# Optimization experiments

Measured on AMD Instinct MI355X. Metric: run time of the kernel, lower is better.

## Reference

```python
import jax, jax.numpy as jnp
import numpy as np

N_NODES = 100000
N_EDGES = 2000000
F_IN = 32
HID = 32
N_CLASS = 40


def _gru_cell(m, h, wih, whh, bih, bhh):
    # torch.nn.GRUCell math; wih/whh: [3H, H_in], gates ordered r, z, n
    gi = m @ wih.T + bih
    gh = h @ whh.T + bhh
    i_r, i_z, i_n = jnp.split(gi, 3, axis=-1)
    h_r, h_z, h_n = jnp.split(gh, 3, axis=-1)
    r = jax.nn.sigmoid(i_r + h_r)
    z = jax.nn.sigmoid(i_z + h_z)
    n = jnp.tanh(i_n + r * h_n)
    return (1.0 - z) * n + z * h


def _gated_conv(x, edge_index, edge_weight, w_proj, w_msg, wih, whh, bih, bhh):
    h = x @ w_proj                                   # [N, out]
    msg = (h @ w_msg)[edge_index[0]] * edge_weight[:, None]  # gather src -> [E, out]
    agg = jax.ops.segment_sum(msg, edge_index[1], num_segments=N_NODES)  # scatter-add to dst
    return _gru_cell(agg, h, wih, whh, bih, bhh)


def setup_inputs() -> dict:
    key = jax.random.key(0)
    ks = jax.random.split(key, 16)
    s = 0.1
    return {
        "x": jax.random.normal(ks[0], (N_NODES, F_IN), jnp.float32),
        "edge_index": jax.random.randint(ks[1], (2, N_EDGES), 0, N_NODES, jnp.int64),
        "edge_weight": jax.random.uniform(ks[2], (N_EDGES,), jnp.float32),
        "W1_proj": jax.random.normal(ks[3], (F_IN, HID), jnp.float32) * s,
        "W1_msg": jax.random.normal(ks[4], (HID, HID), jnp.float32) * s,
        "gru1_wih": jax.random.normal(ks[5], (3 * HID, HID), jnp.float32) * s,
        "gru1_whh": jax.random.normal(ks[6], (3 * HID, HID), jnp.float32) * s,
        "gru1_bih": jax.random.normal(ks[7], (3 * HID,), jnp.float32) * s,
        "gru1_bhh": jax.random.normal(ks[8], (3 * HID,), jnp.float32) * s,
        "W2_proj": jax.random.normal(ks[9], (HID, N_CLASS), jnp.float32) * s,
        "W2_msg": jax.random.normal(ks[10], (N_CLASS, N_CLASS), jnp.float32) * s,
        "gru2_wih": jax.random.normal(ks[11], (3 * N_CLASS, N_CLASS), jnp.float32) * s,
        "gru2_whh": jax.random.normal(ks[12], (3 * N_CLASS, N_CLASS), jnp.float32) * s,
        "gru2_bih": jax.random.normal(ks[13], (3 * N_CLASS,), jnp.float32) * s,
        "gru2_bhh": jax.random.normal(ks[14], (3 * N_CLASS,), jnp.float32) * s,
    }


def reference(x, edge_index, edge_weight, W1_proj, W1_msg, gru1_wih, gru1_whh,
              gru1_bih, gru1_bhh, W2_proj, W2_msg, gru2_wih, gru2_whh,
              gru2_bih, gru2_bhh):
    # eval mode: dropout is identity
    h = _gated_conv(x, edge_index, edge_weight, W1_proj, W1_msg,
                    gru1_wih, gru1_whh, gru1_bih, gru1_bhh)
    h = jax.nn.relu(h)
    h = _gated_conv(h, edge_index, edge_weight, W2_proj, W2_msg,
                    gru2_wih, gru2_whh, gru2_bih, gru2_bhh)
    return jax.nn.log_softmax(h, axis=-1)
```

## Files before the change

### kernel.cpp

```cpp
#include <hip/hip_runtime.h>
#include <math.h>

#define NN 100000
#define NP 100032
#define NE 2000000
#define FIN 32
#define H 32
#define NC 40

#define NBK 196
#define BSH 9
#define CAP 11264
#define EPT 16
#define EPB (256 * EPT)

typedef _Float16 half_t;
typedef __attribute__((ext_vector_type(8))) _Float16 half8;
typedef __attribute__((ext_vector_type(4))) float f32x4;

__device__ __forceinline__ float sigm_(float x) {
    return 1.0f / (1.0f + __expf(-x));
}
__device__ __forceinline__ float tanh_(float x) {
    x = fminf(fmaxf(x, -20.0f), 20.0f);
    float e = __expf(2.0f * x);
    return (e - 1.0f) / (e + 1.0f);
}

__global__ __launch_bounds__(256) void kA_bucket(const int* __restrict__ ei,
                                                 const float* __restrict__ ew,
                                                 int* __restrict__ gcur,
                                                 long long* __restrict__ rec) {
    __shared__ long long recs[EPB];
    __shared__ int gdst[EPB];
    __shared__ int cnt[NBK], base[NBK], sofs[NBK];
    __shared__ int ssc[256];
    int tid = threadIdx.x;
    for (int i = tid; i < NBK; i += 256) cnt[i] = 0;
    __syncthreads();
    int e0 = blockIdx.x * EPB;
    int dcache[EPT];
#pragma unroll
    for (int i = 0; i < EPT; ++i) {
        int e = e0 + i * 256 + tid;
        dcache[i] = (e < NE) ? ei[NE + e] : -1;
        if (e < NE) atomicAdd(&cnt[dcache[i] >> BSH], 1);
    }
    __syncthreads();
    int cv = (tid < NBK) ? cnt[tid] : 0;
    ssc[tid] = cv;
    __syncthreads();
    for (int off = 1; off < 256; off <<= 1) {
        int v = (tid >= off) ? ssc[tid - off] : 0;
        __syncthreads();
        ssc[tid] += v;
        __syncthreads();
    }
    if (tid < NBK) {
        sofs[tid] = ssc[tid] - cv;
        base[tid] = atomicAdd(&gcur[tid], cv);
        cnt[tid] = 0;
    }
    __syncthreads();
#pragma unroll
    for (int i = 0; i < EPT; ++i) {
        int e = e0 + i * 256 + tid;
        if (e < NE) {
            int d = dcache[i], s = ei[e];
            int b = d >> BSH;
            int r = atomicAdd(&cnt[b], 1);
            int slot = sofs[b] + r;
            int pos = base[b] + r;
            int lo = s | ((d & 511) << 17);
            recs[slot] = (long long)(unsigned)lo |
                         ((long long)__float_as_int(ew[e]) << 32);
            gdst[slot] = (pos < CAP) ? (b * CAP + pos) : -1;
        }
    }
    __syncthreads();
    int nrec = min(EPB, NE - e0);
    for (int i = tid; i < nrec; i += 256) {
        int gd = gdst[i];
        if (gd >= 0) rec[gd] = recs[i];
    }
}

__global__ __launch_bounds__(256) void kB_sort(const int* __restrict__ gcur,
                                               const int2* __restrict__ rec,
                                               int2* __restrict__ evs,
                                               int* __restrict__ ofs,
                                               int* __restrict__ ocn) {
    __shared__ int hist[512], lofs[512], ssc[256];
    int tid = threadIdx.x, b = blockIdx.x;
    int nb0 = b << BSH;
    int nnodes = min(512, NN - nb0);
    int cntb = min(gcur[b], CAP);
    hist[tid] = 0;
    hist[tid + 256] = 0;
    __syncthreads();
    const int2* rb = rec + (size_t)b * CAP;
    for (int i = tid; i < cntb; i += 256)
        atomicAdd(&hist[(rb[i].x >> 17) & 511], 1);
    __syncthreads();
    int ps = hist[2 * tid] + hist[2 * tid + 1];
    ssc[tid] = ps;
    __syncthreads();
    for (int off = 1; off < 256; off <<= 1) {
        int v = (tid >= off) ? ssc[tid - off] : 0;
        __syncthreads();
        ssc[tid] += v;
        __syncthreads();
    }
    int ex = ssc[tid] - ps;
    lofs[2 * tid] = ex;
    lofs[2 * tid + 1] = ex + hist[2 * tid];
    __syncthreads();
    for (int l = tid; l < nnodes; l += 256) {
        ofs[nb0 + l] = b * CAP + lofs[l];
        ocn[nb0 + l] = hist[l];
    }
    hist[tid] = 0;
    hist[tid + 256] = 0;
    __syncthreads();
    int2* eb = evs + (size_t)b * CAP;
    for (int i = tid; i < cntb; i += 256) {
        int2 r = rb[i];
        int dl = (r.x >> 17) & 511;
        int rk = atomicAdd(&hist[dl], 1);
        eb[lofs[dl] + rk] = make_int2(r.x & 0x1FFFF, r.y);
    }
}

__global__ __launch_bounds__(256) void k_wpre(const float* __restrict__ W2m,
                                              const float* __restrict__ wih2,
                                              float* __restrict__ M2) {
    int i = blockIdx.x * 256 + threadIdx.x;
    if (i >= NC * 3 * NC) return;
    int u = i / (3 * NC), col = i % (3 * NC);
    float acc = 0.f;
#pragma unroll
    for (int t = 0; t < NC; ++t) acc += W2m[u * NC + t] * wih2[col * NC + t];
    M2[i] = acc;
}

__global__ __launch_bounds__(256) void k_wc(const float* __restrict__ W1m,
                                            const float* __restrict__ wih1,
                                            const float* __restrict__ W2p,
                                            const float* __restrict__ M2,
                                            const float* __restrict__ whh1,
                                            const float* __restrict__ whh2,
                                            half_t* __restrict__ W1sw,
                                            half_t* __restrict__ W2sw) {
    int i = blockIdx.x * 256 + threadIdx.x;
    if (i < 8192) {
        int j = i & 7, lane = (i >> 3) & 63, ct = (i >> 9) & 7, s = i >> 12;
        int k = s * 32 + (lane >> 4) * 8 + j;
        int col = ct * 16 + (lane & 15);
        int g = col >> 5, jj = col & 31;
        float v = 0.f;
        if (g <= 2) {
            if (k < 32) {
                float acc = 0.f;
#pragma unroll
                for (int t = 0; t < H; ++t) acc += W1m[k * H + t] * wih1[(g * H + jj) * H + t];
                v = acc;
            } else if (g < 2) {
                v = whh1[(g * H + jj) * H + (k - 32)];
            }
        } else {
            if (k >= 32) v = whh1[(2 * H + jj) * H + (k - 32)];
        }
        W1sw[i] = (half_t)v;
    } else if (i < 8192 + 18432) {
        int i2 = i - 8192;
        int j = i2 & 7, lane = (i2 >> 3) & 63;
        int tt = i2 >> 9;
        int ct = tt % 12, s = tt / 12;
        int k = s * 32 + (lane >> 4) * 8 + j;
        int col = ct * 16 + (lane & 15);
        int g = col / 48, jj = col % 48;
        float v = 0.f;
        if (jj < NC) {
            if (g <= 2) {
                if (k < 32) {
                    float acc = 0.f;
#pragma unroll
                    for (int u = 0; u < NC; ++u)
                        acc += W2p[k * NC + u] * M2[u * 3 * NC + g * NC + jj];
                    v = acc;
                } else if (k < 72 && g < 2) {
                    v = whh2[(g * NC + jj) * NC + (k - 32)];
                }
            } else {
                if (k >= 32 && k < 72) v = whh2[(2 * NC + jj) * NC + (k - 32)];
            }
        }
        W2sw[i2] = (half_t)v;
    }
}

__global__ __launch_bounds__(256) void k1_proj(const float* __restrict__ x,
                                               const float* __restrict__ Wp,
                                               half_t* __restrict__ Xc1) {
    __shared__ float sWp[FIN * H];
    __shared__ float sx[8][FIN];
    int tid = threadIdx.x;
    for (int i = tid; i < FIN * H; i += 256) sWp[i] = Wp[i];
    int nb = blockIdx.x * 8;
    int nl = tid >> 5, j = tid & 31;
    int n = nb + nl;
    if (n < NN) sx[nl][j] = x[(size_t)n * FIN + j];
    __syncthreads();
    float acc = 0.f;
#pragma unroll
    for (int k = 0; k < FIN; ++k) acc += sx[nl][k] * sWp[k * H + j];
    if (n < NN) Xc1[(size_t)n * 64 + 32 + j] = (half_t)acc;
}

__global__ __launch_bounds__(320) void k4_proj2(const half_t* __restrict__ Hh,
                                                const float* __restrict__ Wp,
                                                half_t* __restrict__ Xc2) {
    __shared__ float sWp[FIN * NC];
    __shared__ float shn[8][FIN];
    int tid = threadIdx.x;
    for (int i = tid; i < FIN * NC; i += 320) sWp[i] = Wp[i];
    int nb = blockIdx.x * 8;
    if (tid < 256) {
        int r = tid >> 5, c = tid & 31;
        shn[r][c] = (float)Hh[(size_t)(nb + r) * 32 + c];
    }
    if (tid < 192) {
        int r = tid / 24, c = tid % 24;
        Xc2[(size_t)(nb + r) * 96 + 72 + c] = (half_t)0.f;
    }
    __syncthreads();
    int nl = tid / NC, j = tid % NC;
    int n = nb + nl;
    float acc = 0.f;
#pragma unroll
    for (int k = 0; k < FIN; ++k) acc += shn[nl][k] * sWp[k * NC + j];
    if (n < NN) Xc2[(size_t)n * 96 + 32 + j] = (half_t)acc;
}

__global__ __launch_bounds__(256) void k_aggh(const int* __restrict__ ofs,
                                              const int* __restrict__ ocn,
                                              const int2* __restrict__ evs,
                                              const half_t* __restrict__ src, int sstr8,
                                              half_t* __restrict__ dst, int dstr) {
    int idx = blockIdx.x * 256 + threadIdx.x;
    int n = idx >> 2, q = idx & 3;
    if (n >= NN) return;
    const half8* s8 = (const half8*)src;
    int s0 = ofs[n], c = ocn[n];
    int e1 = s0 + c;
    float acc[8] = {0.f, 0.f, 0.f, 0.f, 0.f, 0.f, 0.f, 0.f};
    int e = s0;
    for (; e + 4 <= e1; e += 4) {
        int2 r0 = evs[e], r1 = evs[e + 1], r2 = evs[e + 2], r3 = evs[e + 3];
        half8 h0 = s8[(size_t)(r0.x & 0x1FFFF) * sstr8 + q];
        half8 h1 = s8[(size_t)(r1.x & 0x1FFFF) * sstr8 + q];
        half8 h2 = s8[(size_t)(r2.x & 0x1FFFF) * sstr8 + q];
        half8 h3 = s8[(size_t)(r3.x & 0x1FFFF) * sstr8 + q];
        float w0 = __int_as_float(r0.y), w1 = __int_as_float(r1.y);
        float w2 = __int_as_float(r2.y), w3 = __int_as_float(r3.y);
#pragma unroll
        for (int t = 0; t < 8; ++t) {
            acc[t] += w0 * (float)h0[t];
            acc[t] += w1 * (float)h1[t];
            acc[t] += w2 * (float)h2[t];
            acc[t] += w3 * (float)h3[t];
        }
    }
    for (; e < e1; ++e) {
        int2 r = evs[e];
        float w = __int_as_float(r.y);
        half8 hv = s8[(size_t)(r.x & 0x1FFFF) * sstr8 + q];
#pragma unroll
        for (int t = 0; t < 8; ++t) acc[t] += w * (float)hv[t];
    }
    half8 o;
#pragma unroll
    for (int t = 0; t < 8; ++t) o[t] = (half_t)acc[t];
    *(half8*)(dst + (size_t)n * dstr + q * 8) = o;
}

__global__ __launch_bounds__(256) void k3m(const half_t* __restrict__ Xc1,
                                           const half8* __restrict__ W1sw,
                                           const float* __restrict__ bih,
                                           const float* __restrict__ bhh,
                                           half_t* __restrict__ Hh) {
    int tid = threadIdx.x;
    int wave = tid >> 6, lane = tid & 63;
    int m16 = lane & 15, q = lane >> 4;
    int nb = blockIdx.x * 64 + wave * 16;
    const half8* xr = (const half8*)(Xc1 + (size_t)(nb + m16) * 64);
    half8 a0 = xr[q];
    half8 a1 = xr[4 + q];
    f32x4 acc[8];
#pragma unroll
    for (int ct = 0; ct < 8; ++ct) acc[ct] = (f32x4){0.f, 0.f, 0.f, 0.f};
#pragma unroll
    for (int ct = 0; ct < 8; ++ct) {
        acc[ct] = __builtin_amdgcn_mfma_f32_16x16x32_f16(a0, W1sw[ct * 64 + lane], acc[ct], 0, 0, 0);
        acc[ct] = __builtin_amdgcn_mfma_f32_16x16x32_f16(a1, W1sw[(8 + ct) * 64 + lane], acc[ct], 0, 0, 0);
    }
#pragma unroll
    for (int ct = 0; ct < 2; ++ct) {
        int j = ct * 16 + m16;
        float br = bih[j] + bhh[j];
        float bz = bih[H + j] + bhh[H + j];
        float bi = bih[2 * H + j], bh = bhh[2 * H + j];
#pragma unroll
        for (int m = 0; m < 4; ++m) {
            int node = nb + q * 4 + m;
            float r = sigm_(acc[ct][m] + br);
            float z = sigm_(acc[2 + ct][m] + bz);
            float ng = tanh_(acc[4 + ct][m] + bi + r * (acc[6 + ct][m] + bh));
            float hj = (float)Xc1[(size_t)node * 64 + 32 + j];
            float o = fmaxf((1.f - z) * ng + z * hj, 0.f);
            if (node < NN) Hh[(size_t)node * 32 + j] = (half_t)o;
        }
    }
}

__global__ __launch_bounds__(256) void k6m(const half_t* __restrict__ Xc2,
                                           const half8* __restrict__ W2sw,
                                           const float* __restrict__ bih,
                                           const float* __restrict__ bhh,
                                           float* __restrict__ out) {
    int tid = threadIdx.x;
    int wave = tid >> 6, lane = tid & 63;
    int m16 = lane & 15, q = lane >> 4;
    int nb = blockIdx.x * 64 + wave * 16;
    const half8* xr = (const half8*)(Xc2 + (size_t)(nb + m16) * 96);
    half8 a0 = xr[q], a1 = xr[4 + q], a2 = xr[8 + q];
    f32x4 acc[12];
#pragma unroll
    for (int ct = 0; ct < 12; ++ct) acc[ct] = (f32x4){0.f, 0.f, 0.f, 0.f};
#pragma unroll
    for (int ct = 0; ct < 12; ++ct) {
        acc[ct] = __builtin_amdgcn_mfma_f32_16x16x32_f16(a0, W2sw[ct * 64 + lane], acc[ct], 0, 0, 0);
        acc[ct] = __builtin_amdgcn_mfma_f32_16x16x32_f16(a1, W2sw[(12 + ct) * 64 + lane], acc[ct], 0, 0, 0);
        acc[ct] = __builtin_amdgcn_mfma_f32_16x16x32_f16(a2, W2sw[(24 + ct) * 64 + lane], acc[ct], 0, 0, 0);
    }
    float v[3][4];
#pragma unroll
    for (int ct = 0; ct < 3; ++ct) {
        int j = ct * 16 + m16;
        int jc = (j < NC) ? j : (NC - 1);
        float br = bih[jc] + bhh[jc];
        float bz = bih[NC + jc] + bhh[NC + jc];
        float bi = bih[2 * NC + jc], bh = bhh[2 * NC + jc];
#pragma unroll
        for (int m = 0; m < 4; ++m) {
            int node = nb + q * 4 + m;
            float r = sigm_(acc[ct][m] + br);
            float z = sigm_(acc[3 + ct][m] + bz);
            float ng = tanh_(acc[6 + ct][m] + bi + r * (acc[9 + ct][m] + bh));
            float hj = (float)Xc2[(size_t)node * 96 + 32 + jc];
            v[ct][m] = (1.f - z) * ng + z * hj;
        }
    }
    bool v2ok = (m16 < 8);
#pragma unroll
    for (int m = 0; m < 4; ++m) {
        float mx = fmaxf(v[0][m], v[1][m]);
        if (v2ok) mx = fmaxf(mx, v[2][m]);
#pragma unroll
        for (int d = 1; d < 16; d <<= 1) mx = fmaxf(mx, __shfl_xor(mx, d));
        float se = __expf(v[0][m] - mx) + __expf(v[1][m] - mx) +
                   (v2ok ? __expf(v[2][m] - mx) : 0.f);
#pragma unroll
        for (int d = 1; d < 16; d <<= 1) se += __shfl_xor(se, d);
        float ls = mx + __logf(se);
        int node = nb + q * 4 + m;
        if (node < NN) {
            out[(size_t)node * NC + m16] = v[0][m] - ls;
            out[(size_t)node * NC + 16 + m16] = v[1][m] - ls;
            if (v2ok) out[(size_t)node * NC + 32 + m16] = v[2][m] - ls;
        }
    }
}

extern "C" void kernel_launch(void* const* d_in, const int* in_sizes, int n_in,
                              void* d_out, int out_size, void* d_ws, size_t ws_size,
                              hipStream_t stream) {
    const float* x = (const float*)d_in[0];
    const int* ei = (const int*)d_in[1];
    const float* ew = (const float*)d_in[2];
    const float* W1p = (const float*)d_in[3];
    const float* W1m = (const float*)d_in[4];
    const float* g1wih = (const float*)d_in[5];
    const float* g1whh = (const float*)d_in[6];
    const float* g1bih = (const float*)d_in[7];
    const float* g1bhh = (const float*)d_in[8];
    const float* W2p = (const float*)d_in[9];
    const float* W2m = (const float*)d_in[10];
    const float* g2wih = (const float*)d_in[11];
    const float* g2whh = (const float*)d_in[12];
    const float* g2bih = (const float*)d_in[13];
    const float* g2bhh = (const float*)d_in[14];
    float* ws = (float*)d_ws;

    half_t* Xc = (half_t*)ws;
    half_t* Hh = (half_t*)(ws + 4801536);
    int2* rec = (int2*)ws;
    int2* evs = (int2*)(ws + 6402048);
    int* ofs = (int*)(ws + 10817536);
    int* ocn = (int*)(ws + 10917536);
    int* gcur = (int*)(ws + 11017536);
    half_t* W1sw = (half_t*)(ws + 11017792);
    half_t* W2sw = W1sw + 8192;
    float* M2 = ws + 11031104;
    float* out = (float*)d_out;

    hipMemsetAsync(gcur, 0, NBK * sizeof(int), stream);
    kA_bucket<<<(NE + EPB - 1) / EPB, 256, 0, stream>>>(ei, ew, gcur, (long long*)rec);
    kB_sort<<<NBK, 256, 0, stream>>>(gcur, rec, evs, ofs, ocn);
    k_wpre<<<(NC * 3 * NC + 255) / 256, 256, 0, stream>>>(W2m, g2wih, M2);
    k_wc<<<(8192 + 18432 + 255) / 256, 256, 0, stream>>>(
        W1m, g1wih, W2p, M2, g1whh, g2whh, W1sw, W2sw);

    k1_proj<<<NN / 8, 256, 0, stream>>>(x, W1p, Xc);
    k_aggh<<<(NN * 4 + 255) / 256, 256, 0, stream>>>(ofs, ocn, evs, Xc + 32, 8, Xc, 64);
    k3m<<<NP / 64, 256, 0, stream>>>(Xc, (const half8*)W1sw, g1bih, g1bhh, Hh);

    k4_proj2<<<NN / 8, 320, 0, stream>>>(Hh, W2p, Xc);
    k_aggh<<<(NN * 4 + 255) / 256, 256, 0, stream>>>(ofs, ocn, evs, Hh, 4, Xc, 96);
    k6m<<<NP / 64, 256, 0, stream>>>(Xc, (const half8*)W2sw, g2bih, g2bhh, out);
}
```

Measured before the change: 306.0 us.

## Split aggregation across 8 lanes per node with half4 gathers and fold memset

The gather-aggregate kernel now gives each node 8 threads that each handle 4 half features, instead of 4 threads with 8 features each. This doubles thread-level parallelism and the number of in-flight memory requests per node. Edge records are read with nontemporal 64-bit loads, and the strides are now template constants. The memset of the bucket counters is folded into the weight-precompute kernel, which now runs first, removing a separate memset operation. The trade-off is that each edge record is loaded redundantly by twice as many lanes, and each gather is narrower.

Measured after the change: 313.2 us. +2.3%, slower.

```diff
diff --git a/kernel.cpp b/kernel.cpp
--- a/kernel.cpp
+++ b/kernel.cpp
@@ -16,6 +16,7 @@
 
 typedef _Float16 half_t;
 typedef __attribute__((ext_vector_type(8))) _Float16 half8;
+typedef __attribute__((ext_vector_type(4))) _Float16 half4;
 typedef __attribute__((ext_vector_type(4))) float f32x4;
 
 __device__ __forceinline__ float sigm_(float x) {
@@ -133,8 +134,10 @@
 
 __global__ __launch_bounds__(256) void k_wpre(const float* __restrict__ W2m,
                                               const float* __restrict__ wih2,
-                                              float* __restrict__ M2) {
+                                              float* __restrict__ M2,
+                                              int* __restrict__ gcur) {
     int i = blockIdx.x * 256 + threadIdx.x;
+    if (i < NBK) gcur[i] = 0;
     if (i >= NC * 3 * NC) return;
     int u = i / (3 * NC), col = i % (3 * NC);
     float acc = 0.f;
@@ -242,29 +245,36 @@
     if (n < NN) Xc2[(size_t)n * 96 + 32 + j] = (half_t)acc;
 }
 
+template <int SSTR4, int DSTR>
 __global__ __launch_bounds__(256) void k_aggh(const int* __restrict__ ofs,
                                               const int* __restrict__ ocn,
                                               const int2* __restrict__ evs,
-                                              const half_t* __restrict__ src, int sstr8,
-                                              half_t* __restrict__ dst, int dstr) {
+                                              const half_t* __restrict__ src,
+                                              half_t* __restrict__ dst) {
     int idx = blockIdx.x * 256 + threadIdx.x;
-    int n = idx >> 2, q = idx & 3;
+    int n = idx >> 3, q = idx & 7;
     if (n >= NN) return;
-    const half8* s8 = (const half8*)src;
+    const half4* s4 = (const half4*)src + q;
+    const long long* ev8 = (const long long*)evs;
     int s0 = ofs[n], c = ocn[n];
     int e1 = s0 + c;
-    float acc[8] = {0.f, 0.f, 0.f, 0.f, 0.f, 0.f, 0.f, 0.f};
+    float acc[4] = {0.f, 0.f, 0.f, 0.f};
     int e = s0;
     for (; e + 4 <= e1; e += 4) {
-        int2 r0 = evs[e], r1 = evs[e + 1], r2 = evs[e + 2], r3 = evs[e + 3];
-        half8 h0 = s8[(size_t)(r0.x & 0x1FFFF) * sstr8 + q];
-        half8 h1 = s8[(size_t)(r1.x & 0x1FFFF) * sstr8 + q];
-        half8 h2 = s8[(size_t)(r2.x & 0x1FFFF) * sstr8 + q];
-        half8 h3 = s8[(size_t)(r3.x & 0x1FFFF) * sstr8 + q];
-        float w0 = __int_as_float(r0.y), w1 = __int_as_float(r1.y);
-        float w2 = __int_as_float(r2.y), w3 = __int_as_float(r3.y);
-#pragma unroll
-        for (int t = 0; t < 8; ++t) {
+        long long r0 = __builtin_nontemporal_load(ev8 + e);
+        long long r1 = __builtin_nontemporal_load(ev8 + e + 1);
+        long long r2 = __builtin_nontemporal_load(ev8 + e + 2);
+        long long r3 = __builtin_nontemporal_load(ev8 + e + 3);
+        half4 h0 = s4[(size_t)(r0 & 0x1FFFF) * SSTR4];
+        half4 h1 = s4[(size_t)(r1 & 0x1FFFF) * SSTR4];
+        half4 h2 = s4[(size_t)(r2 & 0x1FFFF) * SSTR4];
+        half4 h3 = s4[(size_t)(r3 & 0x1FFFF) * SSTR4];
+        float w0 = __int_as_float((int)(r0 >> 32));
+        float w1 = __int_as_float((int)(r1 >> 32));
+        float w2 = __int_as_float((int)(r2 >> 32));
+        float w3 = __int_as_float((int)(r3 >> 32));
+#pragma unroll
+        for (int t = 0; t < 4; ++t) {
             acc[t] += w0 * (float)h0[t];
             acc[t] += w1 * (float)h1[t];
             acc[t] += w2 * (float)h2[t];
@@ -272,16 +282,16 @@
         }
     }
     for (; e < e1; ++e) {
-        int2 r = evs[e];
-        float w = __int_as_float(r.y);
-        half8 hv = s8[(size_t)(r.x & 0x1FFFF) * sstr8 + q];
-#pragma unroll
-        for (int t = 0; t < 8; ++t) acc[t] += w * (float)hv[t];
-    }
-    half8 o;
-#pragma unroll
-    for (int t = 0; t < 8; ++t) o[t] = (half_t)acc[t];
-    *(half8*)(dst + (size_t)n * dstr + q * 8) = o;
+        long long r = __builtin_nontemporal_load(ev8 + e);
+        float w = __int_as_float((int)(r >> 32));
+        half4 hv = s4[(size_t)(r & 0x1FFFF) * SSTR4];
+#pragma unroll
+        for (int t = 0; t < 4; ++t) acc[t] += w * (float)hv[t];
+    }
+    half4 o;
+#pragma unroll
+    for (int t = 0; t < 4; ++t) o[t] = (half_t)acc[t];
+    *(half4*)(dst + (size_t)n * DSTR + q * 4) = o;
 }
 
 __global__ __launch_bounds__(256) void k3m(const half_t* __restrict__ Xc1,
@@ -414,18 +424,17 @@
     float* M2 = ws + 11031104;
     float* out = (float*)d_out;
 
-    hipMemsetAsync(gcur, 0, NBK * sizeof(int), stream);
+    k_wpre<<<(NC * 3 * NC + 255) / 256, 256, 0, stream>>>(W2m, g2wih, M2, gcur);
     kA_bucket<<<(NE + EPB - 1) / EPB, 256, 0, stream>>>(ei, ew, gcur, (long long*)rec);
     kB_sort<<<NBK, 256, 0, stream>>>(gcur, rec, evs, ofs, ocn);
-    k_wpre<<<(NC * 3 * NC + 255) / 256, 256, 0, stream>>>(W2m, g2wih, M2);
     k_wc<<<(8192 + 18432 + 255) / 256, 256, 0, stream>>>(
         W1m, g1wih, W2p, M2, g1whh, g2whh, W1sw, W2sw);
 
     k1_proj<<<NN / 8, 256, 0, stream>>>(x, W1p, Xc);
-    k_aggh<<<(NN * 4 + 255) / 256, 256, 0, stream>>>(ofs, ocn, evs, Xc + 32, 8, Xc, 64);
+    k_aggh<16, 64><<<(NN * 8 + 255) / 256, 256, 0, stream>>>(ofs, ocn, evs, Xc + 32, Xc);
     k3m<<<NP / 64, 256, 0, stream>>>(Xc, (const half8*)W1sw, g1bih, g1bhh, Hh);
 
     k4_proj2<<<NN / 8, 320, 0, stream>>>(Hh, W2p, Xc);
-    k_aggh<<<(NN * 4 + 255) / 256, 256, 0, stream>>>(ofs, ocn, evs, Hh, 4, Xc, 96);
+    k_aggh<8, 96><<<(NN * 8 + 255) / 256, 256, 0, stream>>>(ofs, ocn, evs, Hh, Xc);
     k6m<<<NP / 64, 256, 0, stream>>>(Xc, (const half8*)W2sw, g2bih, g2bhh, out);
 }
```
